# Optimization experiments

Hardware: AMD Instinct MI355X
Metric: run time of the kernel (lower is better)

The kernel has to match this reference:

```python
import jax, jax.numpy as jnp
import numpy as np

B, N = 256, 512          # trees, nodes per tree (topological order, root last)
IN, HID, OUT = 57, 512, 57  # len(ascii_letters + " .,;'") = 57


def setup_inputs() -> dict:
    rng = np.random.default_rng(0)
    # children indices strictly less than node index; -1 means absent child
    u = rng.random((B, N, 2))
    idx = np.arange(N)[None, :, None]
    ch = np.floor(u * (idx + 1)).astype(np.int32) - 1  # in [-1, i-1]
    left_idx = jnp.asarray(ch[..., 0])
    right_idx = jnp.asarray(ch[..., 1])
    values = jnp.asarray(rng.integers(0, IN, (B, N)), dtype=jnp.int32)
    key = jax.random.key(0)
    k1, k2, k3, k4 = jax.random.split(key, 4)
    s1 = 1.0 / np.sqrt(IN + HID)
    s2 = 1.0 / np.sqrt(HID)
    W_ih = jax.random.uniform(k1, (IN + HID, HID), minval=-s1, maxval=s1, dtype=jnp.float32)
    b_ih = jax.random.uniform(k2, (HID,), minval=-s1, maxval=s1, dtype=jnp.float32)
    W_o = jax.random.uniform(k3, (HID, OUT), minval=-s2, maxval=s2, dtype=jnp.float32)
    b_o = jax.random.uniform(k4, (OUT,), minval=-s2, maxval=s2, dtype=jnp.float32)
    return dict(left_idx=left_idx, right_idx=right_idx, values=values,
                W_ih=W_ih, b_ih=b_ih, W_o=W_o, b_o=b_o)


def _encode(left_idx, right_idx, values, W_ih, b_ih):
    # one-hot chars, precompute the input half of the concat+linear for all nodes
    X = jax.nn.one_hot(values, IN, dtype=W_ih.dtype)        # [B,N,IN]
    Wx, Wh = W_ih[:IN], W_ih[IN:]                            # split concat linear
    Xp = jnp.einsum('bni,ih->bnh', X, Wx) + b_ih             # [B,N,HID]
    SENT = N  # sentinel row holding zeros (hidden for None child)
    li = jnp.where(left_idx < 0, SENT, left_idx)             # [B,N]
    ri = jnp.where(right_idx < 0, SENT, right_idx)
    H0 = jnp.zeros((B, N + 1, HID), Xp.dtype)
    brange = jnp.arange(B)

    def step(H, inp):
        i, xp, l, r = inp                                    # xp:[B,HID], l/r:[B]
        hl = H[brange, l]                                    # gather child hiddens
        hr = H[brange, r]
        h = jnp.tanh(xp + (hl + hr) @ Wh)                    # recurrence
        H = H.at[:, i].set(h)
        return H, None

    xs = (jnp.arange(N), jnp.swapaxes(Xp, 0, 1), li.T, ri.T)
    H, _ = jax.lax.scan(step, H0, xs)
    return H[:, N - 1]                                       # root hidden [B,HID]


def reference(left_idx, right_idx, values, W_ih, b_ih, W_o, b_o):
    h_root = _encode(left_idx, right_idx, values, W_ih, b_ih)
    logits = h_root @ W_o + b_o                              # i2o
    return jax.nn.log_softmax(logits, axis=1)                # [B,OUT]
```

## Files before the change

kernel.cpp:

```cpp
#include <hip/hip_runtime.h>
#include <stdint.h>

#define BATCH 256
#define NNODE 512
#define INP   57
#define HIDD  512
#define OUTD  57

typedef int i32x4 __attribute__((ext_vector_type(4)));

#define MFMA8(ACC, A, B) \
  asm("v_mfma_i32_16x16x64_i8 %0, %1, %2, %0" : "+v"(ACC) : "v"(A), "a"(B))

__device__ __forceinline__ void gload_lds16(const void* g, void* l){
  __builtin_amdgcn_global_load_lds(
      (const __attribute__((address_space(1))) unsigned int*)g,
      (__attribute__((address_space(3))) unsigned int*)l, 16, 0, 0);
}

__global__ void pack_wq(const float* __restrict__ W_ih, const float* __restrict__ b_ih,
                        signed char* __restrict__ Wq){
  int idx = blockIdx.x * 256 + threadIdx.x;
  int j    =  idx        & 15;
  int lane = (idx >> 4)  & 63;
  int nt   = (idx >> 10) & 31;
  int kt   =  idx >> 15;
  int n    = nt * 16 + (lane & 15);
  int ksub = (lane >> 4) * 16 + j;
  const float scale = 127.0f * sqrtf((float)(INP + HIDD));
  float wv;
  if (kt < 8)            wv = W_ih[(size_t)(INP + kt * 64 + ksub) * HIDD + n];
  else if (ksub < INP)   wv = W_ih[(size_t)ksub * HIDD + n];
  else if (ksub == INP)  wv = b_ih[n];
  else                   wv = 0.0f;
  float q = rintf(wv * scale);
  q = fminf(127.0f, fmaxf(-127.0f, q));
  Wq[idx] = (signed char)q;
}

template<int NMT>
__device__ __forceinline__ void chunk_body(
    int m0, int Mcur, int w, int lane, int m16, int quad,
    signed char* __restrict__ Al, signed char* __restrict__ Ar,
    const int* ord_s, const int* li_s, const int* ri_s, const int* val_s,
    const i32x4 (&Bv)[9][2],
    signed char* Hb)
{
  {
    int kt, mt; bool doL, doR;
    if constexpr (NMT == 2) { kt = w >> 1; mt = w & 1; doL = true;    doR = true;  }
    else                    { kt = w & 7;  mt = 0;     doL = (w < 8); doR = (w >= 8); }
    const int row  = mt * 16 + m16;
    const int node = (row < Mcur) ? ord_s[m0 + row] : -1;
    const size_t koff = (size_t)kt * 64 + quad * 16;
    if (doL) {
      int l = (node >= 0) ? li_s[node] : -1;
      gload_lds16(Hb + (size_t)(l < 0 ? NNODE : l) * HIDD + koff,
                  Al + (kt * 2 + mt) * 1024);
    }
    if (doR) {
      int r = (node >= 0) ? ri_s[node] : -1;
      gload_lds16(Hb + (size_t)(r < 0 ? NNODE : r) * HIDD + koff,
                  Ar + (kt * 2 + mt) * 1024);
    }
    if (w < NMT) {
      const int erow  = w * 16 + m16;
      const int enode = (erow < Mcur) ? ord_s[m0 + erow] : -1;
      const int v     = (enode >= 0) ? val_s[enode] : -1;
      signed char bytes[16];
      #pragma unroll
      for (int j = 0; j < 16; ++j) {
        const int ks = quad * 16 + j;
        bytes[j] = (enode >= 0 && (ks == v || ks == INP)) ? (signed char)127 : (signed char)0;
      }
      *(i32x4*)(Al + (16 + w) * 1024 + lane * 16) = *(const i32x4*)bytes;
    }
  }
  __syncthreads();

  i32x4 acc[NMT][2];
  #pragma unroll
  for (int mt = 0; mt < NMT; ++mt)
    #pragma unroll
    for (int nt = 0; nt < 2; ++nt)
      acc[mt][nt] = (i32x4){0, 0, 0, 0};

  #pragma unroll
  for (int kt = 0; kt < 8; ++kt) {
    #pragma unroll
    for (int mt = 0; mt < NMT; ++mt) {
      i32x4 al = *(const i32x4*)(Al + (kt * 2 + mt) * 1024 + lane * 16);
      i32x4 ar = *(const i32x4*)(Ar + (kt * 2 + mt) * 1024 + lane * 16);
      MFMA8(acc[mt][0], al, Bv[kt][0]);
      MFMA8(acc[mt][1], al, Bv[kt][1]);
      MFMA8(acc[mt][0], ar, Bv[kt][0]);
      MFMA8(acc[mt][1], ar, Bv[kt][1]);
    }
  }
  #pragma unroll
  for (int mt = 0; mt < NMT; ++mt) {
    i32x4 ax = *(const i32x4*)(Al + (16 + mt) * 1024 + lane * 16);
    MFMA8(acc[mt][0], ax, Bv[8][0]);
    MFMA8(acc[mt][1], ax, Bv[8][1]);
  }

  const float SCL2 = 2.0f / (16129.0f * sqrtf((float)(INP + HIDD)));
  #pragma unroll
  for (int nt = 0; nt < 2; ++nt) {
    const int col = (w * 2 + nt) * 16 + m16;
    #pragma unroll
    for (int mt = 0; mt < NMT; ++mt) {
      #pragma unroll
      for (int rg = 0; rg < 4; ++rg) {
        const int rowc = mt * 16 + quad * 4 + rg;
        if (rowc < Mcur) {
          const int node = ord_s[m0 + rowc];
          const float e  = __expf((float)acc[mt][nt][rg] * SCL2);
          const float tq = 127.0f - __fdividef(254.0f, e + 1.0f);
          Hb[(size_t)node * HIDD + col] = (signed char)__float2int_rn(tq);
        }
      }
    }
  }
  __syncthreads();
}

__global__ __launch_bounds__(1024) void tree_rnn(
    const int* __restrict__ left, const int* __restrict__ right,
    const int* __restrict__ values,
    const float* __restrict__ W_ih, const float* __restrict__ b_ih,
    const float* __restrict__ W_o,  const float* __restrict__ b_o,
    const signed char* __restrict__ Wq,
    signed char* __restrict__ Hbuf, float* __restrict__ out)
{
  __shared__ __align__(16) signed char Al_s[18 * 1024];
  __shared__ __align__(16) signed char Ar_s[16 * 1024];
  __shared__ int li_s[NNODE], ri_s[NNODE], val_s[NNODE];
  __shared__ int lvl_s[NNODE], ord_s[NNODE];
  __shared__ int cnt_s[NNODE], cnt2_s[NNODE];
  __shared__ int offs_s[NNODE + 1];
  __shared__ int chg_s, lmax_s;
  __shared__ float hroot_s[HIDD];
  __shared__ float red_s[OUTD][16];
  __shared__ float logit_s[64];

  const int b    = blockIdx.x;
  const int tid  = threadIdx.x;
  const int lane = tid & 63;
  const int w    = tid >> 6;
  signed char* Hb = Hbuf + (size_t)b * (NNODE + 1) * HIDD;

  if (tid < NNODE) {
    li_s[tid]  = left  [b * NNODE + tid];
    ri_s[tid]  = right [b * NNODE + tid];
    val_s[tid] = values[b * NNODE + tid];
    lvl_s[tid] = 0; cnt_s[tid] = 0; cnt2_s[tid] = 0;
  }
  if (tid < 128) ((unsigned int*)(Hb + (size_t)NNODE * HIDD))[tid] = 0;
  if (tid == 0) lmax_s = 0;
  __syncthreads();

  for (;;) {
    if (tid == 0) chg_s = 0;
    __syncthreads();
    if (tid < NNODE) {
      int l = li_s[tid], r = ri_s[tid];
      int dl = (l >= 0) ? lvl_s[l] : -1;
      int dr = (r >= 0) ? lvl_s[r] : -1;
      int nl = 1 + (dl > dr ? dl : dr);
      if (nl > lvl_s[tid]) { lvl_s[tid] = nl; chg_s = 1; }
    }
    __syncthreads();
    if (!chg_s) break;
  }

  int myl = 0;
  if (tid < NNODE) {
    myl = lvl_s[tid];
    int ml = myl;
    #pragma unroll
    for (int m = 1; m < 64; m <<= 1) ml = max(ml, __shfl_xor(ml, m, 64));
    if (lane == 0) atomicMax(&lmax_s, ml);
    atomicAdd(&cnt_s[myl], 1);
  }
  __syncthreads();
  const int Lmax = lmax_s;
  if (tid == 0) {
    int acc = 0;
    for (int L = 0; L <= Lmax; ++L) { offs_s[L] = acc; acc += cnt_s[L]; }
    offs_s[Lmax + 1] = acc;
  }
  __syncthreads();
  if (tid < NNODE) {
    int pos = offs_s[myl] + atomicAdd(&cnt2_s[myl], 1);
    ord_s[pos] = tid;
  }
  __syncthreads();

  const int m16  = lane & 15;
  const int quad = lane >> 4;

  i32x4 Bv[9][2];
  #pragma unroll
  for (int kt = 0; kt < 9; ++kt)
    #pragma unroll
    for (int nt = 0; nt < 2; ++nt)
      Bv[kt][nt] = *(const i32x4*)(Wq + ((size_t)(kt * 32 + 2 * w + nt) * 64 + lane) * 16);

  for (int L = 0; L <= Lmax; ++L) {
    const int start = offs_s[L], end = offs_s[L + 1];
    for (int m0 = start; m0 < end; m0 += 32) {
      const int Mcur = min(32, end - m0);
      if (Mcur > 16)
        chunk_body<2>(m0, Mcur, w, lane, m16, quad, Al_s, Ar_s,
                      ord_s, li_s, ri_s, val_s, Bv, Hb);
      else
        chunk_body<1>(m0, Mcur, w, lane, m16, quad, Al_s, Ar_s,
                      ord_s, li_s, ri_s, val_s, Bv, Hb);
    }
  }

  if (tid < HIDD)
    hroot_s[tid] = (float)Hb[(size_t)(NNODE - 1) * HIDD + tid] * (1.0f / 127.0f);
  __syncthreads();
  {
    const int j = tid >> 4, part = tid & 15;
    if (j < OUTD) {
      float p = 0.f;
      const int k0 = part * 32;
      for (int k = k0; k < k0 + 32; ++k)
        p += hroot_s[k] * W_o[(size_t)k * OUTD + j];
      red_s[j][part] = p;
    }
  }
  __syncthreads();
  if (tid < OUTD) {
    float s = b_o[tid];
    #pragma unroll
    for (int p = 0; p < 16; ++p) s += red_s[tid][p];
    logit_s[tid] = s;
  }
  __syncthreads();
  if (w == 0) {
    float x = (lane < OUTD) ? logit_s[lane] : -1e30f;
    float mx = x;
    #pragma unroll
    for (int m = 1; m < 64; m <<= 1) mx = fmaxf(mx, __shfl_xor(mx, m, 64));
    float ex = (lane < OUTD) ? __expf(x - mx) : 0.f;
    float sm = ex;
    #pragma unroll
    for (int m = 1; m < 64; m <<= 1) sm += __shfl_xor(sm, m, 64);
    float ls = logf(sm);
    if (lane < OUTD) out[b * OUTD + lane] = x - mx - ls;
  }
}

extern "C" void kernel_launch(void* const* d_in, const int* in_sizes, int n_in,
                              void* d_out, int out_size, void* d_ws, size_t ws_size,
                              hipStream_t stream) {
  const int*   left   = (const int*)  d_in[0];
  const int*   right  = (const int*)  d_in[1];
  const int*   values = (const int*)  d_in[2];
  const float* W_ih   = (const float*)d_in[3];
  const float* b_ih   = (const float*)d_in[4];
  const float* W_o    = (const float*)d_in[5];
  const float* b_o    = (const float*)d_in[6];
  float* out = (float*)d_out;

  signed char* Wq   = (signed char*)d_ws;
  signed char* Hbuf = (signed char*)((char*)d_ws + 512 * 1024);

  pack_wq<<<1152, 256, 0, stream>>>(W_ih, b_ih, Wq);
  tree_rnn<<<BATCH, 1024, 0, stream>>>(left, right, values, W_ih, b_ih, W_o, b_o,
                                       Wq, Hbuf, out);
}
```

Baseline: 239.5 us.

## Halve workgroup to 512 threads with four N-tiles per wave, two blocks per CU

```diff
diff --git a/kernel.cpp b/kernel.cpp
--- a/kernel.cpp
+++ b/kernel.cpp
@@ -8,9 +8,6 @@
 #define OUTD  57
 
 typedef int i32x4 __attribute__((ext_vector_type(4)));
-
-#define MFMA8(ACC, A, B) \
-  asm("v_mfma_i32_16x16x64_i8 %0, %1, %2, %0" : "+v"(ACC) : "v"(A), "a"(B))
 
 __device__ __forceinline__ void gload_lds16(const void* g, void* l){
   __builtin_amdgcn_global_load_lds(
@@ -43,23 +40,20 @@
     int m0, int Mcur, int w, int lane, int m16, int quad,
     signed char* __restrict__ Al, signed char* __restrict__ Ar,
     const int* ord_s, const int* li_s, const int* ri_s, const int* val_s,
-    const i32x4 (&Bv)[9][2],
+    const i32x4 (&Bv)[9][4],
     signed char* Hb)
 {
   {
-    int kt, mt; bool doL, doR;
-    if constexpr (NMT == 2) { kt = w >> 1; mt = w & 1; doL = true;    doR = true;  }
-    else                    { kt = w & 7;  mt = 0;     doL = (w < 8); doR = (w >= 8); }
-    const int row  = mt * 16 + m16;
-    const int node = (row < Mcur) ? ord_s[m0 + row] : -1;
+    const int kt = w;
     const size_t koff = (size_t)kt * 64 + quad * 16;
-    if (doL) {
-      int l = (node >= 0) ? li_s[node] : -1;
+    #pragma unroll
+    for (int mt = 0; mt < NMT; ++mt) {
+      const int row  = mt * 16 + m16;
+      const int node = (row < Mcur) ? ord_s[m0 + row] : -1;
+      const int l = (node >= 0) ? li_s[node] : -1;
       gload_lds16(Hb + (size_t)(l < 0 ? NNODE : l) * HIDD + koff,
                   Al + (kt * 2 + mt) * 1024);
-    }
-    if (doR) {
-      int r = (node >= 0) ? ri_s[node] : -1;
+      const int r = (node >= 0) ? ri_s[node] : -1;
       gload_lds16(Hb + (size_t)(r < 0 ? NNODE : r) * HIDD + koff,
                   Ar + (kt * 2 + mt) * 1024);
     }
@@ -78,11 +72,11 @@
   }
   __syncthreads();
 
-  i32x4 acc[NMT][2];
+  i32x4 acc[NMT][4];
   #pragma unroll
   for (int mt = 0; mt < NMT; ++mt)
     #pragma unroll
-    for (int nt = 0; nt < 2; ++nt)
+    for (int nt = 0; nt < 4; ++nt)
       acc[mt][nt] = (i32x4){0, 0, 0, 0};
 
   #pragma unroll
@@ -90,24 +84,27 @@
     #pragma unroll
     for (int mt = 0; mt < NMT; ++mt) {
       i32x4 al = *(const i32x4*)(Al + (kt * 2 + mt) * 1024 + lane * 16);
+      #pragma unroll
+      for (int nt = 0; nt < 4; ++nt)
+        acc[mt][nt] = __builtin_amdgcn_mfma_i32_16x16x64_i8(al, Bv[kt][nt], acc[mt][nt], 0, 0, 0);
       i32x4 ar = *(const i32x4*)(Ar + (kt * 2 + mt) * 1024 + lane * 16);
-      MFMA8(acc[mt][0], al, Bv[kt][0]);
-      MFMA8(acc[mt][1], al, Bv[kt][1]);
-      MFMA8(acc[mt][0], ar, Bv[kt][0]);
-      MFMA8(acc[mt][1], ar, Bv[kt][1]);
+      #pragma unroll
+      for (int nt = 0; nt < 4; ++nt)
+        acc[mt][nt] = __builtin_amdgcn_mfma_i32_16x16x64_i8(ar, Bv[kt][nt], acc[mt][nt], 0, 0, 0);
     }
   }
   #pragma unroll
   for (int mt = 0; mt < NMT; ++mt) {
     i32x4 ax = *(const i32x4*)(Al + (16 + mt) * 1024 + lane * 16);
-    MFMA8(acc[mt][0], ax, Bv[8][0]);
-    MFMA8(acc[mt][1], ax, Bv[8][1]);
+    #pragma unroll
+    for (int nt = 0; nt < 4; ++nt)
+      acc[mt][nt] = __builtin_amdgcn_mfma_i32_16x16x64_i8(ax, Bv[8][nt], acc[mt][nt], 0, 0, 0);
   }
 
   const float SCL2 = 2.0f / (16129.0f * sqrtf((float)(INP + HIDD)));
   #pragma unroll
-  for (int nt = 0; nt < 2; ++nt) {
-    const int col = (w * 2 + nt) * 16 + m16;
+  for (int nt = 0; nt < 4; ++nt) {
+    const int col = (w * 4 + nt) * 16 + m16;
     #pragma unroll
     for (int mt = 0; mt < NMT; ++mt) {
       #pragma unroll
@@ -125,7 +122,7 @@
   __syncthreads();
 }
 
-__global__ __launch_bounds__(1024) void tree_rnn(
+__global__ __launch_bounds__(512, 2) void tree_rnn(
     const int* __restrict__ left, const int* __restrict__ right,
     const int* __restrict__ values,
     const float* __restrict__ W_ih, const float* __restrict__ b_ih,
@@ -141,7 +138,7 @@
   __shared__ int offs_s[NNODE + 1];
   __shared__ int chg_s, lmax_s;
   __shared__ float hroot_s[HIDD];
-  __shared__ float red_s[OUTD][16];
+  __shared__ float red_s[OUTD][8];
   __shared__ float logit_s[64];
 
   const int b    = blockIdx.x;
@@ -150,12 +147,10 @@
   const int w    = tid >> 6;
   signed char* Hb = Hbuf + (size_t)b * (NNODE + 1) * HIDD;
 
-  if (tid < NNODE) {
-    li_s[tid]  = left  [b * NNODE + tid];
-    ri_s[tid]  = right [b * NNODE + tid];
-    val_s[tid] = values[b * NNODE + tid];
-    lvl_s[tid] = 0; cnt_s[tid] = 0; cnt2_s[tid] = 0;
-  }
+  li_s[tid]  = left  [b * NNODE + tid];
+  ri_s[tid]  = right [b * NNODE + tid];
+  val_s[tid] = values[b * NNODE + tid];
+  lvl_s[tid] = 0; cnt_s[tid] = 0; cnt2_s[tid] = 0;
   if (tid < 128) ((unsigned int*)(Hb + (size_t)NNODE * HIDD))[tid] = 0;
   if (tid == 0) lmax_s = 0;
   __syncthreads();
@@ -163,7 +158,7 @@
   for (;;) {
     if (tid == 0) chg_s = 0;
     __syncthreads();
-    if (tid < NNODE) {
+    {
       int l = li_s[tid], r = ri_s[tid];
       int dl = (l >= 0) ? lvl_s[l] : -1;
       int dr = (r >= 0) ? lvl_s[r] : -1;
@@ -174,9 +169,8 @@
     if (!chg_s) break;
   }
 
-  int myl = 0;
-  if (tid < NNODE) {
-    myl = lvl_s[tid];
+  const int myl = lvl_s[tid];
+  {
     int ml = myl;
     #pragma unroll
     for (int m = 1; m < 64; m <<= 1) ml = max(ml, __shfl_xor(ml, m, 64));
@@ -191,7 +185,7 @@
     offs_s[Lmax + 1] = acc;
   }
   __syncthreads();
-  if (tid < NNODE) {
+  {
     int pos = offs_s[myl] + atomicAdd(&cnt2_s[myl], 1);
     ord_s[pos] = tid;
   }
@@ -200,12 +194,12 @@
   const int m16  = lane & 15;
   const int quad = lane >> 4;
 
-  i32x4 Bv[9][2];
+  i32x4 Bv[9][4];
   #pragma unroll
   for (int kt = 0; kt < 9; ++kt)
     #pragma unroll
-    for (int nt = 0; nt < 2; ++nt)
-      Bv[kt][nt] = *(const i32x4*)(Wq + ((size_t)(kt * 32 + 2 * w + nt) * 64 + lane) * 16);
+    for (int nt = 0; nt < 4; ++nt)
+      Bv[kt][nt] = *(const i32x4*)(Wq + ((size_t)(kt * 32 + 4 * w + nt) * 64 + lane) * 16);
 
   for (int L = 0; L <= Lmax; ++L) {
     const int start = offs_s[L], end = offs_s[L + 1];
@@ -220,15 +214,14 @@
     }
   }
 
-  if (tid < HIDD)
-    hroot_s[tid] = (float)Hb[(size_t)(NNODE - 1) * HIDD + tid] * (1.0f / 127.0f);
-  __syncthreads();
-  {
-    const int j = tid >> 4, part = tid & 15;
+  hroot_s[tid] = (float)Hb[(size_t)(NNODE - 1) * HIDD + tid] * (1.0f / 127.0f);
+  __syncthreads();
+  {
+    const int j = tid >> 3, part = tid & 7;
     if (j < OUTD) {
       float p = 0.f;
-      const int k0 = part * 32;
-      for (int k = k0; k < k0 + 32; ++k)
+      const int k0 = part * 64;
+      for (int k = k0; k < k0 + 64; ++k)
         p += hroot_s[k] * W_o[(size_t)k * OUTD + j];
       red_s[j][part] = p;
     }
@@ -237,7 +230,7 @@
   if (tid < OUTD) {
     float s = b_o[tid];
     #pragma unroll
-    for (int p = 0; p < 16; ++p) s += red_s[tid][p];
+    for (int p = 0; p < 8; ++p) s += red_s[tid][p];
     logit_s[tid] = s;
   }
   __syncthreads();
@@ -271,6 +264,6 @@
   signed char* Hbuf = (signed char*)((char*)d_ws + 512 * 1024);
 
   pack_wq<<<1152, 256, 0, stream>>>(W_ih, b_ih, Wq);
-  tree_rnn<<<BATCH, 1024, 0, stream>>>(left, right, values, W_ih, b_ih, W_o, b_o,
-                                       Wq, Hbuf, out);
-}
+  tree_rnn<<<BATCH, 512, 0, stream>>>(left, right, values, W_ih, b_ih, W_o, b_o,
+                                      Wq, Hbuf, out);
+}
```

Result: no change. 236.7 us (-1.2%).
